# Kernel optimization log

Hardware: AMD Instinct MI355X
Metric: run time of the kernel (lower is better)

## Reference

```python
import jax, jax.numpy as jnp
import numpy as np

B, T, H, LAT, ADIM = 8192, 40, 100, 10, 2
ATT_TEMP = 5.0


def setup_inputs() -> dict:
    key = jax.random.key(0)
    ks = jax.random.split(key, 12)
    return {
        "sampled_att_z": jax.random.normal(ks[0], (B, LAT), jnp.float32),
        "enc_h": jax.random.normal(ks[1], (B, H), jnp.float32),
        # keep IDM params strictly positive / physically plausible to avoid inf
        "idm_params": 1.0 + 2.0 * jax.random.uniform(ks[2], (B, 5), jnp.float32),
        "idm_s": jax.random.uniform(ks[3], (B, T, 8), jnp.float32),
        "sdv_acts": jax.random.normal(ks[4], (B, T, ADIM), jnp.float32),
        "linear_W": jax.random.normal(ks[5], (LAT, H), jnp.float32) / np.float32(np.sqrt(LAT)),
        "linear_b": jnp.zeros((H,), jnp.float32),
        "lstm_Wx": jax.random.normal(ks[6], (H + ADIM, 4 * H), jnp.float32) / np.float32(np.sqrt(H + ADIM)),
        "lstm_Wh": jax.random.normal(ks[7], (H, 4 * H), jnp.float32) / np.float32(np.sqrt(H)),
        "lstm_b": jnp.zeros((4 * H,), jnp.float32),
        "att_W": jax.random.normal(ks[8], (H, 1), jnp.float32) / np.float32(np.sqrt(H)),
        "att_b": jnp.zeros((1,), jnp.float32),
        # precomputed per-step noise, replacing tf.random.normal inside the loop
        "noise_f": jax.random.normal(ks[9], (T, B, 1), jnp.float32),
        "noise_m": jax.random.normal(ks[10], (T, B, 1), jnp.float32),
    }


def reference(sampled_att_z, enc_h, idm_params, idm_s, sdv_acts,
              linear_W, linear_b, lstm_Wx, lstm_Wh, lstm_b, att_W, att_b,
              noise_f, noise_m):
    desired_v = idm_params[:, 0:1]
    desired_tgap = idm_params[:, 1:2]
    min_jamx = idm_params[:, 2:3]
    max_act = idm_params[:, 3:4]
    min_act = idm_params[:, 4:5]

    def idm_driver(vel, dv, dx):  # all [B,1]
        dx = jnp.clip(dx, 0.5, 1000.0)
        desired_gap = min_jamx + jax.nn.relu(
            desired_tgap * vel + vel * dv / (2.0 * jnp.sqrt(max_act * min_act)))
        act = max_act * (1.0 - (vel / desired_v) ** 4 - (desired_gap / dx) ** 2)
        return jnp.clip(act, -3.0, 3.0)

    att_proj = sampled_att_z @ linear_W + linear_b  # [B,H]; also the att_context and init h,c

    s_tm = jnp.swapaxes(idm_s, 0, 1)      # [T,B,8]
    a_tm = jnp.swapaxes(sdv_acts, 0, 1)   # [T,B,ADIM]

    ego_v0 = idm_s[:, 0, 0:1]
    ego_x0 = idm_s[:, 0, 3:4]
    zero_act = jnp.zeros_like(ego_v0)  # step-0 kinematic update is a no-op

    def step(carry, xs):
        ego_v, ego_x, h, c, act = carry
        s, sdv, nf, nm = xs
        ego_v = ego_v + act * 0.1
        ego_x = ego_x + ego_v * 0.1 + 0.5 * act * 0.1 ** 2

        f_v, m_v = s[:, 1:2], s[:, 2:3]
        f_x, m_x = s[:, 4:5], s[:, 5:6]
        f_ex, m_ex = s[:, 6:7], s[:, 7:8]

        ef_act = idm_driver(ego_v, ego_v - f_v, f_x - ego_x)
        ef_act = f_ex * ef_act + (1.0 - f_ex) * nf
        em_act = idm_driver(ego_v, ego_v - m_v, m_x - ego_x)
        em_act = m_ex * em_act + (1.0 - m_ex) * nm

        x_in = jnp.concatenate([att_proj, sdv], axis=-1)  # [B,H+ADIM]
        z = x_in @ lstm_Wx + h @ lstm_Wh + lstm_b          # [B,4H], keras gate order i,f,g,o
        zi, zf, zg, zo = jnp.split(z, 4, axis=-1)
        c = jax.nn.sigmoid(zf) * c + jax.nn.sigmoid(zi) * jnp.tanh(zg)
        h = jax.nn.sigmoid(zo) * jnp.tanh(c)

        att_score = jax.nn.sigmoid(ATT_TEMP * (h @ att_W + att_b))  # [B,1]
        act = (1.0 - att_score) * ef_act + att_score * em_act
        return (ego_v, ego_x, h, c, act), (act, att_score)

    init = (ego_v0, ego_x0, att_proj, att_proj, zero_act)
    _, (acts, atts) = jax.lax.scan(step, init, (s_tm, a_tm, noise_f, noise_m))
    act_seq = jnp.swapaxes(acts, 0, 1)  # [B,T,1]
    att_seq = jnp.swapaxes(atts, 0, 1)  # [B,T,1]
    return act_seq, att_seq
```

## Files before the change

### kernel.cpp

```cpp
#include <hip/hip_runtime.h>
#include <math.h>


#define B_TOT 8192
#define T_STEPS 40
#define NB 16

typedef _Float16 f16;
typedef f16 f16x8 __attribute__((ext_vector_type(8)));
typedef float f32x4 __attribute__((ext_vector_type(4)));

__device__ __forceinline__ float rcpf(float x) { return __builtin_amdgcn_rcpf(x); }
__device__ __forceinline__ float ex2(float x)  { return __builtin_amdgcn_exp2f(x); }
__device__ __forceinline__ float sigf(float x)  { return rcpf(1.f + ex2(-1.44269504f * x)); }
__device__ __forceinline__ float tanhf_(float x){ return fmaf(-2.f, rcpf(1.f + ex2(2.88539008f * x)), 1.f); }


__global__ __launch_bounds__(256) void idm_prep(
    const float* __restrict__ Wx, const float* __restrict__ Wh,
    const float* __restrict__ bvec, const float* __restrict__ attw,
    f16* __restrict__ whb, f16* __restrict__ wxb,
    float* __restrict__ bp, f16* __restrict__ awb)
{
  int i = blockIdx.x * 256 + threadIdx.x;
  int k = i >> 9, n = i & 511;
  int g = n >> 7, j128 = n & 127;
  float vh = 0.f, vx = 0.f;
  if (j128 < 100) {
    int col = g * 100 + j128;
    if (k < 100)      { vh = Wh[k * 400 + col]; vx = Wx[k * 400 + col]; }
    else if (k < 102) { vh = Wx[k * 400 + col]; }
  }
  int idx = (((n >> 4) * 4 + (k >> 5)) * 64 + (((k >> 3) & 3) * 16 + (n & 15))) * 8 + (k & 7);
  whb[idx] = (f16)vh;
  wxb[idx] = (f16)vx;
  if (i < 512) { int gg = i >> 7, jj = i & 127; bp[i] = (jj < 100) ? bvec[gg * 100 + jj] : 0.f; }
  if (i < 2048) {
    int j = i & 7, l = (i >> 3) & 63, kf = i >> 9;
    int kk = kf * 32 + ((l >> 4) & 3) * 8 + j;
    int col = l & 15;
    awb[i] = (f16)((col == 0 && kk < 100) ? attw[kk] : 0.f);
  }
}

__global__ __launch_bounds__(448, 4) void idm_main(
    const float* __restrict__ z_att,
    const float* __restrict__ linear_W,
    const float* __restrict__ linear_b,
    const float* __restrict__ sdv_acts,
    const f16* __restrict__ whb, const f16* __restrict__ wxb,
    const float* __restrict__ bp, const f16* __restrict__ awbg,
    const float* __restrict__ idm_params,
    const float* __restrict__ idm_s,
    const float* __restrict__ att_b,
    const float* __restrict__ noise_f,
    const float* __restrict__ noise_m,
    float* __restrict__ out)
{
  __shared__ f16 hS[2][16][136];
  __shared__ f16 sdvS[T_STEPS][16][2];
  __shared__ float logitS[T_STEPS][16];

  const int tid = threadIdx.x;
  const int w  = tid >> 6;
  const int l  = tid & 63;
  const int lr = l & 15;
  const int lq = l >> 4;
  const int b0g = blockIdx.x * NB;
  const int jcol = 16 * w + lr;

  for (int idx = tid; idx < 2176; idx += 448) ((unsigned*)hS)[idx] = 0u;
  for (int idx = tid; idx < 1280; idx += 448) {
    float v = sdv_acts[(size_t)b0g * 80 + idx];
    int b = idx / 80, r = idx - b * 80;
    sdvS[r >> 1][b][r & 1] = (f16)v;
  }
  __syncthreads();

  if (tid < 256) {
    int b = tid >> 4, oct = tid & 15;
    float za[10];
    #pragma unroll
    for (int t2 = 0; t2 < 10; ++t2) za[t2] = z_att[(b0g + b) * 10 + t2];
    #pragma unroll
    for (int jj = 0; jj < 8; ++jj) {
      int j = oct * 8 + jj;
      if (j < 100) {
        float acc = linear_b[j];
        #pragma unroll
        for (int t2 = 0; t2 < 10; ++t2) acc = fmaf(za[t2], linear_W[t2 * 100 + j], acc);
        hS[0][b][j] = (f16)acc;
      }
    }
  }
  if (tid < 32) {
    int bb = tid >> 1, ii = tid & 1;
    hS[0][bb][100 + ii] = sdvS[0][bb][ii];
  }
  __syncthreads();

  f16x8 wb[4][4];
  #pragma unroll
  for (int g = 0; g < 4; ++g) {
    int tile = w + 8 * g;
    #pragma unroll
    for (int kf = 0; kf < 4; ++kf)
      wb[g][kf] = *(const f16x8*)(wxb + ((size_t)(tile * 4 + kf) * 64 + l) * 8);
  }
  f32x4 cx[4];
  #pragma unroll
  for (int g = 0; g < 4; ++g) {
    float bpv = bp[(w + 8 * g) * 16 + lr];
    f32x4 c = {bpv, bpv, bpv, bpv};
    cx[g] = c;
  }
  #pragma unroll
  for (int kf = 0; kf < 4; ++kf) {
    f16x8 a = *(const f16x8*)(&hS[0][lr][kf * 32 + lq * 8]);
    #pragma unroll
    for (int g = 0; g < 4; ++g)
      cx[g] = __builtin_amdgcn_mfma_f32_16x16x32_f16(a, wb[g][kf], cx[g], 0, 0, 0);
  }
  #pragma unroll
  for (int g = 0; g < 4; ++g) {
    int tile = w + 8 * g;
    #pragma unroll
    for (int kf = 0; kf < 4; ++kf)
      wb[g][kf] = *(const f16x8*)(whb + ((size_t)(tile * 4 + kf) * 64 + l) * 8);
  }
  f16x8 awb[4];
  #pragma unroll
  for (int kf = 0; kf < 4; ++kf)
    awb[kf] = *(const f16x8*)(awbg + ((size_t)kf * 64 + l) * 8);

  float cst[4];
  #pragma unroll
  for (int r = 0; r < 4; ++r) cst[r] = (float)hS[0][lq * 4 + r][jcol];

  int p = 0;
  for (int t = 0; t < T_STEPS; ++t) {
    f16x8 a0 = *(const f16x8*)(&hS[p][lr][0  + lq * 8]);
    f16x8 a1 = *(const f16x8*)(&hS[p][lr][32 + lq * 8]);
    f16x8 a2 = *(const f16x8*)(&hS[p][lr][64 + lq * 8]);
    f16x8 a3 = *(const f16x8*)(&hS[p][lr][96 + lq * 8]);
    f32x4 z0 = cx[0], z1 = cx[1], z2 = cx[2], z3 = cx[3];
    z0 = __builtin_amdgcn_mfma_f32_16x16x32_f16(a0, wb[0][0], z0, 0, 0, 0);
    z1 = __builtin_amdgcn_mfma_f32_16x16x32_f16(a0, wb[1][0], z1, 0, 0, 0);
    z2 = __builtin_amdgcn_mfma_f32_16x16x32_f16(a0, wb[2][0], z2, 0, 0, 0);
    z3 = __builtin_amdgcn_mfma_f32_16x16x32_f16(a0, wb[3][0], z3, 0, 0, 0);
    z0 = __builtin_amdgcn_mfma_f32_16x16x32_f16(a1, wb[0][1], z0, 0, 0, 0);
    z1 = __builtin_amdgcn_mfma_f32_16x16x32_f16(a1, wb[1][1], z1, 0, 0, 0);
    z2 = __builtin_amdgcn_mfma_f32_16x16x32_f16(a1, wb[2][1], z2, 0, 0, 0);
    z3 = __builtin_amdgcn_mfma_f32_16x16x32_f16(a1, wb[3][1], z3, 0, 0, 0);
    z0 = __builtin_amdgcn_mfma_f32_16x16x32_f16(a2, wb[0][2], z0, 0, 0, 0);
    z1 = __builtin_amdgcn_mfma_f32_16x16x32_f16(a2, wb[1][2], z1, 0, 0, 0);
    z2 = __builtin_amdgcn_mfma_f32_16x16x32_f16(a2, wb[2][2], z2, 0, 0, 0);
    z3 = __builtin_amdgcn_mfma_f32_16x16x32_f16(a2, wb[3][2], z3, 0, 0, 0);
    z0 = __builtin_amdgcn_mfma_f32_16x16x32_f16(a3, wb[0][3], z0, 0, 0, 0);
    z1 = __builtin_amdgcn_mfma_f32_16x16x32_f16(a3, wb[1][3], z1, 0, 0, 0);
    z2 = __builtin_amdgcn_mfma_f32_16x16x32_f16(a3, wb[2][3], z2, 0, 0, 0);
    z3 = __builtin_amdgcn_mfma_f32_16x16x32_f16(a3, wb[3][3], z3, 0, 0, 0);

    if (w == 0) {
      f32x4 zA = {0.f, 0.f, 0.f, 0.f};
      zA = __builtin_amdgcn_mfma_f32_16x16x32_f16(a0, awb[0], zA, 0, 0, 0);
      zA = __builtin_amdgcn_mfma_f32_16x16x32_f16(a1, awb[1], zA, 0, 0, 0);
      zA = __builtin_amdgcn_mfma_f32_16x16x32_f16(a2, awb[2], zA, 0, 0, 0);
      zA = __builtin_amdgcn_mfma_f32_16x16x32_f16(a3, awb[3], zA, 0, 0, 0);
      if (t > 0 && lr == 0) {
        #pragma unroll
        for (int r = 0; r < 4; ++r) logitS[t - 1][lq * 4 + r] = zA[r];
      }
    }

    #pragma unroll
    for (int r = 0; r < 4; ++r) {
      float si = sigf(z0[r]);
      float sf = sigf(z1[r]);
      float tg = tanhf_(z2[r]);
      float so = sigf(z3[r]);
      float cc = fmaf(sf, cst[r], si * tg);
      float hh = so * tanhf_(cc);
      cst[r] = cc;
      if (jcol < 100) hS[p ^ 1][lq * 4 + r][jcol] = (f16)hh;
    }
    if (t + 1 < T_STEPS && tid < 32) {
      int bb = tid >> 1, ii = tid & 1;
      hS[p ^ 1][bb][100 + ii] = sdvS[t + 1][bb][ii];
    }
    __syncthreads();
    p ^= 1;
  }

  if (w == 0) {
    f16x8 a0 = *(const f16x8*)(&hS[p][lr][0  + lq * 8]);
    f16x8 a1 = *(const f16x8*)(&hS[p][lr][32 + lq * 8]);
    f16x8 a2 = *(const f16x8*)(&hS[p][lr][64 + lq * 8]);
    f16x8 a3 = *(const f16x8*)(&hS[p][lr][96 + lq * 8]);
    f32x4 zA = {0.f, 0.f, 0.f, 0.f};
    zA = __builtin_amdgcn_mfma_f32_16x16x32_f16(a0, awb[0], zA, 0, 0, 0);
    zA = __builtin_amdgcn_mfma_f32_16x16x32_f16(a1, awb[1], zA, 0, 0, 0);
    zA = __builtin_amdgcn_mfma_f32_16x16x32_f16(a2, awb[2], zA, 0, 0, 0);
    zA = __builtin_amdgcn_mfma_f32_16x16x32_f16(a3, awb[3], zA, 0, 0, 0);
    if (lr == 0) {
      #pragma unroll
      for (int r = 0; r < 4; ++r) logitS[T_STEPS - 1][lq * 4 + r] = zA[r];
    }
  }
  __syncthreads();

  if (tid < 16) {
    int b = b0g + tid;
    const float* P = idm_params + (size_t)b * 5;
    float des_v = P[0], des_tg = P[1], min_jx = P[2], max_a = P[3];
    float inv2s = 0.5f / sqrtf(max_a * P[4]);
    float inv_dv = rcpf(des_v);
    float ego_v = idm_s[(size_t)b * T_STEPS * 8 + 0];
    float ego_x = idm_s[(size_t)b * T_STEPS * 8 + 3];
    float attb = att_b[0];
    float act = 0.f;
    for (int t = 0; t < T_STEPS; ++t) {
      const float* s = idm_s + ((size_t)b * T_STEPS + t) * 8;
      float4 s03 = *(const float4*)(s);
      float4 s47 = *(const float4*)(s + 4);
      float nf = noise_f[(size_t)t * B_TOT + b];
      float nm = noise_m[(size_t)t * B_TOT + b];
      float lg = attb + logitS[t][tid];

      ego_v += act * 0.1f;
      ego_x += ego_v * 0.1f + act * 0.005f;
      float f_v = s03.y, m_v = s03.z, f_x = s47.x, m_x = s47.y, f_ex = s47.z, m_ex = s47.w;
      float af_, am_;
      {
        float dx = fminf(fmaxf(f_x - ego_x, 0.5f), 1000.f);
        float dg = min_jx + fmaxf(0.f, des_tg * ego_v + ego_v * (ego_v - f_v) * inv2s);
        float r = ego_v * inv_dv; float r2 = r * r; float q = dg * rcpf(dx);
        af_ = fminf(fmaxf(max_a * (1.f - r2 * r2 - q * q), -3.f), 3.f);
      }
      {
        float dx = fminf(fmaxf(m_x - ego_x, 0.5f), 1000.f);
        float dg = min_jx + fmaxf(0.f, des_tg * ego_v + ego_v * (ego_v - m_v) * inv2s);
        float r = ego_v * inv_dv; float r2 = r * r; float q = dg * rcpf(dx);
        am_ = fminf(fmaxf(max_a * (1.f - r2 * r2 - q * q), -3.f), 3.f);
      }
      float ef2 = f_ex * af_ + (1.f - f_ex) * nf;
      float em2 = m_ex * am_ + (1.f - m_ex) * nm;
      float att = sigf(5.f * lg);
      act = (1.f - att) * ef2 + att * em2;
      out[(size_t)b * T_STEPS + t] = act;
      out[(size_t)B_TOT * T_STEPS + (size_t)b * T_STEPS + t] = att;
    }
  }
}

extern "C" void kernel_launch(void* const* d_in, const int* in_sizes, int n_in,
                              void* d_out, int out_size, void* d_ws, size_t ws_size,
                              hipStream_t stream) {
  const float* z_att      = (const float*)d_in[0];
  const float* idm_params = (const float*)d_in[2];
  const float* idm_s      = (const float*)d_in[3];
  const float* sdv_acts   = (const float*)d_in[4];
  const float* linear_W   = (const float*)d_in[5];
  const float* linear_b   = (const float*)d_in[6];
  const float* lstm_Wx    = (const float*)d_in[7];
  const float* lstm_Wh    = (const float*)d_in[8];
  const float* lstm_b     = (const float*)d_in[9];
  const float* att_W      = (const float*)d_in[10];
  const float* att_b      = (const float*)d_in[11];
  const float* noise_f    = (const float*)d_in[12];
  const float* noise_m    = (const float*)d_in[13];
  float* out = (float*)d_out;

  f16*   whb = (f16*)d_ws;
  f16*   wxb = (f16*)((char*)d_ws + 131072);
  float* bp  = (float*)((char*)d_ws + 262144);
  f16*   awb = (f16*)((char*)d_ws + 264192);

  idm_prep<<<256, 256, 0, stream>>>(lstm_Wx, lstm_Wh, lstm_b, att_W, whb, wxb, bp, awb);
  idm_main<<<B_TOT / NB, 448, 0, stream>>>(z_att, linear_W, linear_b, sdv_acts,
                                           whb, wxb, bp, awb,
                                           idm_params, idm_s, att_b,
                                           noise_f, noise_m, out);
}
```

Measured before the change: 192.7 us.

## Split LSTM gate tiles across 14 waves with smem transpose for cell update

Doubles the block to 896 threads so each wave holds two gate tiles instead of four, writes the gate pre-activations to a shared transpose buffer, and lets every thread compute the cell update for one hidden unit across two batch rows. The aim is to cut per-wave serial MFMA and transcendental work inside the 40-step recurrence. The IDM inputs, noise and attention weights are now staged in shared memory, and outputs are written back as coalesced vectors. In exchange there is a second barrier per step, much more LDS use, and a single h buffer in place of the double buffer.

```diff
diff --git a/kernel.cpp b/kernel.cpp
--- a/kernel.cpp
+++ b/kernel.cpp
@@ -43,7 +43,7 @@
   }
 }
 
-__global__ __launch_bounds__(448, 4) void idm_main(
+__global__ __launch_bounds__(896, 7) void idm_main(
     const float* __restrict__ z_att,
     const float* __restrict__ linear_W,
     const float* __restrict__ linear_b,
@@ -57,9 +57,14 @@
     const float* __restrict__ noise_m,
     float* __restrict__ out)
 {
-  __shared__ f16 hS[2][16][136];
-  __shared__ f16 sdvS[T_STEPS][16][2];
+  __shared__ f16   hS[16][136];
+  __shared__ float zT[496][20];
   __shared__ float logitS[T_STEPS][16];
+  __shared__ f16   sdvS[T_STEPS][16][2];
+  __shared__ float sS[16][T_STEPS][6];
+  __shared__ float nS[2][T_STEPS][16];
+  __shared__ float accS[2][16][T_STEPS];
+  __shared__ f16   awbS[2048];
 
   const int tid = threadIdx.x;
   const int w  = tid >> 6;
@@ -67,14 +72,33 @@
   const int lr = l & 15;
   const int lq = l >> 4;
   const int b0g = blockIdx.x * NB;
-  const int jcol = 16 * w + lr;
-
-  for (int idx = tid; idx < 2176; idx += 448) ((unsigned*)hS)[idx] = 0u;
-  for (int idx = tid; idx < 1280; idx += 448) {
+  const int i1 = 2 * w, i2 = 2 * w + 1;
+  const int T1 = (i1 / 7) * 8 + (i1 % 7);
+  const int T2 = (i2 / 7) * 8 + (i2 % 7);
+  const int gj = tid >> 3;
+  const int gb = (tid & 7) * 2;
+
+  for (int idx = tid; idx < 1088; idx += 896) ((unsigned*)hS)[idx] = 0u;
+  for (int idx = tid; idx < 1280; idx += 896) {
     float v = sdv_acts[(size_t)b0g * 80 + idx];
     int b = idx / 80, r = idx - b * 80;
     sdvS[r >> 1][b][r & 1] = (f16)v;
   }
+  for (int idx = tid; idx < 5120; idx += 896) {
+    int f = idx & 7;
+    if (f != 0 && f != 3) {
+      int b = idx / 320, rem = idx - b * 320, t = rem >> 3;
+      sS[b][t][(f < 3) ? f - 1 : f - 2] = idm_s[(size_t)b0g * 320 + idx];
+    }
+  }
+  for (int idx = tid; idx < 1280; idx += 896) {
+    int which = idx >= 640 ? 1 : 0;
+    int r = idx - which * 640;
+    int t = r >> 4, i = r & 15;
+    nS[which][t][i] = which ? noise_m[(size_t)t * B_TOT + b0g + i]
+                            : noise_f[(size_t)t * B_TOT + b0g + i];
+  }
+  for (int idx = tid; idx < 1024; idx += 896) ((unsigned*)awbS)[idx] = ((const unsigned*)awbg)[idx];
   __syncthreads();
 
   if (tid < 256) {
@@ -89,122 +113,89 @@
         float acc = linear_b[j];
         #pragma unroll
         for (int t2 = 0; t2 < 10; ++t2) acc = fmaf(za[t2], linear_W[t2 * 100 + j], acc);
-        hS[0][b][j] = (f16)acc;
-      }
-    }
-  }
-  if (tid < 32) {
-    int bb = tid >> 1, ii = tid & 1;
-    hS[0][bb][100 + ii] = sdvS[0][bb][ii];
-  }
-  __syncthreads();
-
-  f16x8 wb[4][4];
-  #pragma unroll
-  for (int g = 0; g < 4; ++g) {
-    int tile = w + 8 * g;
-    #pragma unroll
-    for (int kf = 0; kf < 4; ++kf)
-      wb[g][kf] = *(const f16x8*)(wxb + ((size_t)(tile * 4 + kf) * 64 + l) * 8);
-  }
-  f32x4 cx[4];
-  #pragma unroll
-  for (int g = 0; g < 4; ++g) {
-    float bpv = bp[(w + 8 * g) * 16 + lr];
-    f32x4 c = {bpv, bpv, bpv, bpv};
-    cx[g] = c;
-  }
+        hS[b][j] = (f16)acc;
+      }
+    }
+  }
+  if (tid < 32) hS[tid >> 1][100 + (tid & 1)] = sdvS[0][tid >> 1][tid & 1];
+  __syncthreads();
+
+  f16x8 wbA[4], wbB[4];
   #pragma unroll
   for (int kf = 0; kf < 4; ++kf) {
-    f16x8 a = *(const f16x8*)(&hS[0][lr][kf * 32 + lq * 8]);
-    #pragma unroll
-    for (int g = 0; g < 4; ++g)
-      cx[g] = __builtin_amdgcn_mfma_f32_16x16x32_f16(a, wb[g][kf], cx[g], 0, 0, 0);
-  }
+    wbA[kf] = *(const f16x8*)(wxb + ((size_t)(T1 * 4 + kf) * 64 + l) * 8);
+    wbB[kf] = *(const f16x8*)(wxb + ((size_t)(T2 * 4 + kf) * 64 + l) * 8);
+  }
+  float bpA = bp[T1 * 16 + lr], bpB = bp[T2 * 16 + lr];
+  f32x4 cxA = {bpA, bpA, bpA, bpA};
+  f32x4 cxB = {bpB, bpB, bpB, bpB};
   #pragma unroll
-  for (int g = 0; g < 4; ++g) {
-    int tile = w + 8 * g;
-    #pragma unroll
-    for (int kf = 0; kf < 4; ++kf)
-      wb[g][kf] = *(const f16x8*)(whb + ((size_t)(tile * 4 + kf) * 64 + l) * 8);
-  }
-  f16x8 awb[4];
+  for (int kf = 0; kf < 4; ++kf) {
+    f16x8 a = *(const f16x8*)(&hS[lr][kf * 32 + lq * 8]);
+    cxA = __builtin_amdgcn_mfma_f32_16x16x32_f16(a, wbA[kf], cxA, 0, 0, 0);
+    cxB = __builtin_amdgcn_mfma_f32_16x16x32_f16(a, wbB[kf], cxB, 0, 0, 0);
+  }
   #pragma unroll
-  for (int kf = 0; kf < 4; ++kf)
-    awb[kf] = *(const f16x8*)(awbg + ((size_t)kf * 64 + l) * 8);
-
-  float cst[4];
-  #pragma unroll
-  for (int r = 0; r < 4; ++r) cst[r] = (float)hS[0][lq * 4 + r][jcol];
-
-  int p = 0;
+  for (int kf = 0; kf < 4; ++kf) {
+    wbA[kf] = *(const f16x8*)(whb + ((size_t)(T1 * 4 + kf) * 64 + l) * 8);
+    wbB[kf] = *(const f16x8*)(whb + ((size_t)(T2 * 4 + kf) * 64 + l) * 8);
+  }
+
+  float cst0 = 0.f, cst1 = 0.f;
+  const bool glive = (gj < 100);
+  if (glive) { cst0 = (float)hS[gb][gj]; cst1 = (float)hS[gb + 1][gj]; }
+
+  #pragma unroll 1
   for (int t = 0; t < T_STEPS; ++t) {
-    f16x8 a0 = *(const f16x8*)(&hS[p][lr][0  + lq * 8]);
-    f16x8 a1 = *(const f16x8*)(&hS[p][lr][32 + lq * 8]);
-    f16x8 a2 = *(const f16x8*)(&hS[p][lr][64 + lq * 8]);
-    f16x8 a3 = *(const f16x8*)(&hS[p][lr][96 + lq * 8]);
-    f32x4 z0 = cx[0], z1 = cx[1], z2 = cx[2], z3 = cx[3];
-    z0 = __builtin_amdgcn_mfma_f32_16x16x32_f16(a0, wb[0][0], z0, 0, 0, 0);
-    z1 = __builtin_amdgcn_mfma_f32_16x16x32_f16(a0, wb[1][0], z1, 0, 0, 0);
-    z2 = __builtin_amdgcn_mfma_f32_16x16x32_f16(a0, wb[2][0], z2, 0, 0, 0);
-    z3 = __builtin_amdgcn_mfma_f32_16x16x32_f16(a0, wb[3][0], z3, 0, 0, 0);
-    z0 = __builtin_amdgcn_mfma_f32_16x16x32_f16(a1, wb[0][1], z0, 0, 0, 0);
-    z1 = __builtin_amdgcn_mfma_f32_16x16x32_f16(a1, wb[1][1], z1, 0, 0, 0);
-    z2 = __builtin_amdgcn_mfma_f32_16x16x32_f16(a1, wb[2][1], z2, 0, 0, 0);
-    z3 = __builtin_amdgcn_mfma_f32_16x16x32_f16(a1, wb[3][1], z3, 0, 0, 0);
-    z0 = __builtin_amdgcn_mfma_f32_16x16x32_f16(a2, wb[0][2], z0, 0, 0, 0);
-    z1 = __builtin_amdgcn_mfma_f32_16x16x32_f16(a2, wb[1][2], z1, 0, 0, 0);
-    z2 = __builtin_amdgcn_mfma_f32_16x16x32_f16(a2, wb[2][2], z2, 0, 0, 0);
-    z3 = __builtin_amdgcn_mfma_f32_16x16x32_f16(a2, wb[3][2], z3, 0, 0, 0);
-    z0 = __builtin_amdgcn_mfma_f32_16x16x32_f16(a3, wb[0][3], z0, 0, 0, 0);
-    z1 = __builtin_amdgcn_mfma_f32_16x16x32_f16(a3, wb[1][3], z1, 0, 0, 0);
-    z2 = __builtin_amdgcn_mfma_f32_16x16x32_f16(a3, wb[2][3], z2, 0, 0, 0);
-    z3 = __builtin_amdgcn_mfma_f32_16x16x32_f16(a3, wb[3][3], z3, 0, 0, 0);
-
-    if (w == 0) {
-      f32x4 zA = {0.f, 0.f, 0.f, 0.f};
-      zA = __builtin_amdgcn_mfma_f32_16x16x32_f16(a0, awb[0], zA, 0, 0, 0);
-      zA = __builtin_amdgcn_mfma_f32_16x16x32_f16(a1, awb[1], zA, 0, 0, 0);
-      zA = __builtin_amdgcn_mfma_f32_16x16x32_f16(a2, awb[2], zA, 0, 0, 0);
-      zA = __builtin_amdgcn_mfma_f32_16x16x32_f16(a3, awb[3], zA, 0, 0, 0);
-      if (t > 0 && lr == 0) {
-        #pragma unroll
-        for (int r = 0; r < 4; ++r) logitS[t - 1][lq * 4 + r] = zA[r];
-      }
-    }
-
-    #pragma unroll
-    for (int r = 0; r < 4; ++r) {
-      float si = sigf(z0[r]);
-      float sf = sigf(z1[r]);
-      float tg = tanhf_(z2[r]);
-      float so = sigf(z3[r]);
-      float cc = fmaf(sf, cst[r], si * tg);
-      float hh = so * tanhf_(cc);
-      cst[r] = cc;
-      if (jcol < 100) hS[p ^ 1][lq * 4 + r][jcol] = (f16)hh;
-    }
-    if (t + 1 < T_STEPS && tid < 32) {
-      int bb = tid >> 1, ii = tid & 1;
-      hS[p ^ 1][bb][100 + ii] = sdvS[t + 1][bb][ii];
-    }
+    f32x4 zA = cxA, zB = cxB;
+    f32x4 zL = {0.f, 0.f, 0.f, 0.f};
+    #pragma unroll
+    for (int kf = 0; kf < 4; ++kf) {
+      f16x8 a = *(const f16x8*)(&hS[lr][kf * 32 + lq * 8]);
+      zA = __builtin_amdgcn_mfma_f32_16x16x32_f16(a, wbA[kf], zA, 0, 0, 0);
+      zB = __builtin_amdgcn_mfma_f32_16x16x32_f16(a, wbB[kf], zB, 0, 0, 0);
+      if (w == 0) {
+        f16x8 af = *(const f16x8*)(awbS + ((size_t)kf * 64 + l) * 8);
+        zL = __builtin_amdgcn_mfma_f32_16x16x32_f16(a, af, zL, 0, 0, 0);
+      }
+    }
+    if (w == 0 && t > 0 && lr == 0) {
+      #pragma unroll
+      for (int r = 0; r < 4; ++r) logitS[t - 1][lq * 4 + r] = zL[r];
+    }
+    *(f32x4*)&zT[T1 * 16 + lr][lq * 4] = zA;
+    *(f32x4*)&zT[T2 * 16 + lr][lq * 4] = zB;
     __syncthreads();
-    p ^= 1;
+
+    if (glive) {
+      float2 zi = *(const float2*)&zT[0 * 128 + gj][gb];
+      float2 zf = *(const float2*)&zT[1 * 128 + gj][gb];
+      float2 zg = *(const float2*)&zT[2 * 128 + gj][gb];
+      float2 zo = *(const float2*)&zT[3 * 128 + gj][gb];
+      float cc0 = fmaf(sigf(zf.x), cst0, sigf(zi.x) * tanhf_(zg.x));
+      float hh0 = sigf(zo.x) * tanhf_(cc0);
+      float cc1 = fmaf(sigf(zf.y), cst1, sigf(zi.y) * tanhf_(zg.y));
+      float hh1 = sigf(zo.y) * tanhf_(cc1);
+      cst0 = cc0; cst1 = cc1;
+      hS[gb][gj]     = (f16)hh0;
+      hS[gb + 1][gj] = (f16)hh1;
+    }
+    if (t + 1 < T_STEPS && tid < 32)
+      hS[tid >> 1][100 + (tid & 1)] = sdvS[t + 1][tid >> 1][tid & 1];
+    __syncthreads();
   }
 
   if (w == 0) {
-    f16x8 a0 = *(const f16x8*)(&hS[p][lr][0  + lq * 8]);
-    f16x8 a1 = *(const f16x8*)(&hS[p][lr][32 + lq * 8]);
-    f16x8 a2 = *(const f16x8*)(&hS[p][lr][64 + lq * 8]);
-    f16x8 a3 = *(const f16x8*)(&hS[p][lr][96 + lq * 8]);
-    f32x4 zA = {0.f, 0.f, 0.f, 0.f};
-    zA = __builtin_amdgcn_mfma_f32_16x16x32_f16(a0, awb[0], zA, 0, 0, 0);
-    zA = __builtin_amdgcn_mfma_f32_16x16x32_f16(a1, awb[1], zA, 0, 0, 0);
-    zA = __builtin_amdgcn_mfma_f32_16x16x32_f16(a2, awb[2], zA, 0, 0, 0);
-    zA = __builtin_amdgcn_mfma_f32_16x16x32_f16(a3, awb[3], zA, 0, 0, 0);
+    f32x4 zL = {0.f, 0.f, 0.f, 0.f};
+    #pragma unroll
+    for (int kf = 0; kf < 4; ++kf) {
+      f16x8 a  = *(const f16x8*)(&hS[lr][kf * 32 + lq * 8]);
+      f16x8 af = *(const f16x8*)(awbS + ((size_t)kf * 64 + l) * 8);
+      zL = __builtin_amdgcn_mfma_f32_16x16x32_f16(a, af, zL, 0, 0, 0);
+    }
     if (lr == 0) {
       #pragma unroll
-      for (int r = 0; r < 4; ++r) logitS[T_STEPS - 1][lq * 4 + r] = zA[r];
+      for (int r = 0; r < 4; ++r) logitS[T_STEPS - 1][lq * 4 + r] = zL[r];
     }
   }
   __syncthreads();
@@ -215,41 +206,47 @@
     float des_v = P[0], des_tg = P[1], min_jx = P[2], max_a = P[3];
     float inv2s = 0.5f / sqrtf(max_a * P[4]);
     float inv_dv = rcpf(des_v);
-    float ego_v = idm_s[(size_t)b * T_STEPS * 8 + 0];
-    float ego_x = idm_s[(size_t)b * T_STEPS * 8 + 3];
+    float ego_v = idm_s[(size_t)b * 320 + 0];
+    float ego_x = idm_s[(size_t)b * 320 + 3];
     float attb = att_b[0];
     float act = 0.f;
+    #pragma unroll 4
     for (int t = 0; t < T_STEPS; ++t) {
-      const float* s = idm_s + ((size_t)b * T_STEPS + t) * 8;
-      float4 s03 = *(const float4*)(s);
-      float4 s47 = *(const float4*)(s + 4);
-      float nf = noise_f[(size_t)t * B_TOT + b];
-      float nm = noise_m[(size_t)t * B_TOT + b];
+      float2 s01 = *(const float2*)&sS[tid][t][0];
+      float2 s23 = *(const float2*)&sS[tid][t][2];
+      float2 s45 = *(const float2*)&sS[tid][t][4];
+      float nf = nS[0][t][tid], nm = nS[1][t][tid];
       float lg = attb + logitS[t][tid];
-
       ego_v += act * 0.1f;
       ego_x += ego_v * 0.1f + act * 0.005f;
-      float f_v = s03.y, m_v = s03.z, f_x = s47.x, m_x = s47.y, f_ex = s47.z, m_ex = s47.w;
       float af_, am_;
       {
-        float dx = fminf(fmaxf(f_x - ego_x, 0.5f), 1000.f);
-        float dg = min_jx + fmaxf(0.f, des_tg * ego_v + ego_v * (ego_v - f_v) * inv2s);
+        float dx = fminf(fmaxf(s23.x - ego_x, 0.5f), 1000.f);
+        float dg = min_jx + fmaxf(0.f, des_tg * ego_v + ego_v * (ego_v - s01.x) * inv2s);
         float r = ego_v * inv_dv; float r2 = r * r; float q = dg * rcpf(dx);
         af_ = fminf(fmaxf(max_a * (1.f - r2 * r2 - q * q), -3.f), 3.f);
       }
       {
-        float dx = fminf(fmaxf(m_x - ego_x, 0.5f), 1000.f);
-        float dg = min_jx + fmaxf(0.f, des_tg * ego_v + ego_v * (ego_v - m_v) * inv2s);
+        float dx = fminf(fmaxf(s23.y - ego_x, 0.5f), 1000.f);
+        float dg = min_jx + fmaxf(0.f, des_tg * ego_v + ego_v * (ego_v - s01.y) * inv2s);
         float r = ego_v * inv_dv; float r2 = r * r; float q = dg * rcpf(dx);
         am_ = fminf(fmaxf(max_a * (1.f - r2 * r2 - q * q), -3.f), 3.f);
       }
-      float ef2 = f_ex * af_ + (1.f - f_ex) * nf;
-      float em2 = m_ex * am_ + (1.f - m_ex) * nm;
+      float ef2 = s45.x * af_ + (1.f - s45.x) * nf;
+      float em2 = s45.y * am_ + (1.f - s45.y) * nm;
       float att = sigf(5.f * lg);
       act = (1.f - att) * ef2 + att * em2;
-      out[(size_t)b * T_STEPS + t] = act;
-      out[(size_t)B_TOT * T_STEPS + (size_t)b * T_STEPS + t] = att;
-    }
+      accS[0][tid][t] = act;
+      accS[1][tid][t] = att;
+    }
+  }
+  __syncthreads();
+
+  if (tid < 160) {
+    f32x4 va = ((const f32x4*)&accS[0][0][0])[tid];
+    f32x4 vt = ((const f32x4*)&accS[1][0][0])[tid];
+    *(f32x4*)(out + (size_t)b0g * T_STEPS + tid * 4) = va;
+    *(f32x4*)(out + (size_t)B_TOT * T_STEPS + (size_t)b0g * T_STEPS + tid * 4) = vt;
   }
 }
 
@@ -277,7 +274,7 @@
   f16*   awb = (f16*)((char*)d_ws + 264192);
 
   idm_prep<<<256, 256, 0, stream>>>(lstm_Wx, lstm_Wh, lstm_b, att_W, whb, wxb, bp, awb);
-  idm_main<<<B_TOT / NB, 448, 0, stream>>>(z_att, linear_W, linear_b, sdv_acts,
+  idm_main<<<B_TOT / NB, 896, 0, stream>>>(z_att, linear_W, linear_b, sdv_acts,
                                            whb, wxb, bp, awb,
                                            idm_params, idm_s, att_b,
                                            noise_f, noise_m, out);
```

After: 245.6 us. +27.5%, slower.

## Fold attention logit into padded gate column and stage IDM inputs in LDS

Applied to the files above, without the earlier changes.

The attention weight vector is packed into an unused padding column (n=100) of the Wh tile, so the logit comes out of the existing gate MFMA for wave 6. This removes the separate per-step attention MFMA chain on wave 0. The IDM state and noise are prefetched cooperatively into shared memory before the recurrence, and outputs are buffered in LDS and written with coalesced vector stores instead of scattered per-thread global stores. The cost is extra LDS use, which may lower occupancy.

```diff
diff --git a/kernel.cpp b/kernel.cpp
--- a/kernel.cpp
+++ b/kernel.cpp
@@ -20,7 +20,7 @@
     const float* __restrict__ Wx, const float* __restrict__ Wh,
     const float* __restrict__ bvec, const float* __restrict__ attw,
     f16* __restrict__ whb, f16* __restrict__ wxb,
-    float* __restrict__ bp, f16* __restrict__ awb)
+    float* __restrict__ bp)
 {
   int i = blockIdx.x * 256 + threadIdx.x;
   int k = i >> 9, n = i & 511;
@@ -30,17 +30,13 @@
     int col = g * 100 + j128;
     if (k < 100)      { vh = Wh[k * 400 + col]; vx = Wx[k * 400 + col]; }
     else if (k < 102) { vh = Wx[k * 400 + col]; }
+  } else if (n == 100 && k < 100) {
+    vh = attw[k];
   }
   int idx = (((n >> 4) * 4 + (k >> 5)) * 64 + (((k >> 3) & 3) * 16 + (n & 15))) * 8 + (k & 7);
   whb[idx] = (f16)vh;
   wxb[idx] = (f16)vx;
   if (i < 512) { int gg = i >> 7, jj = i & 127; bp[i] = (jj < 100) ? bvec[gg * 100 + jj] : 0.f; }
-  if (i < 2048) {
-    int j = i & 7, l = (i >> 3) & 63, kf = i >> 9;
-    int kk = kf * 32 + ((l >> 4) & 3) * 8 + j;
-    int col = l & 15;
-    awb[i] = (f16)((col == 0 && kk < 100) ? attw[kk] : 0.f);
-  }
 }
 
 __global__ __launch_bounds__(448, 4) void idm_main(
@@ -49,7 +45,7 @@
     const float* __restrict__ linear_b,
     const float* __restrict__ sdv_acts,
     const f16* __restrict__ whb, const f16* __restrict__ wxb,
-    const float* __restrict__ bp, const f16* __restrict__ awbg,
+    const float* __restrict__ bp,
     const float* __restrict__ idm_params,
     const float* __restrict__ idm_s,
     const float* __restrict__ att_b,
@@ -57,9 +53,12 @@
     const float* __restrict__ noise_m,
     float* __restrict__ out)
 {
-  __shared__ f16 hS[2][16][136];
-  __shared__ f16 sdvS[T_STEPS][16][2];
+  __shared__ f16   hS[2][16][136];
+  __shared__ f16   sdvS[T_STEPS][16][2];
   __shared__ float logitS[T_STEPS][16];
+  __shared__ float sS[16][T_STEPS][6];
+  __shared__ float nS[2][T_STEPS][16];
+  __shared__ float accS[2][16][T_STEPS];
 
   const int tid = threadIdx.x;
   const int w  = tid >> 6;
@@ -74,6 +73,20 @@
     float v = sdv_acts[(size_t)b0g * 80 + idx];
     int b = idx / 80, r = idx - b * 80;
     sdvS[r >> 1][b][r & 1] = (f16)v;
+  }
+  for (int idx = tid; idx < 5120; idx += 448) {
+    int f = idx & 7;
+    if (f != 0 && f != 3) {
+      int b = idx / 320, rem = idx - b * 320, t = rem >> 3;
+      sS[b][t][(f < 3) ? f - 1 : f - 2] = idm_s[(size_t)b0g * 320 + idx];
+    }
+  }
+  for (int idx = tid; idx < 1280; idx += 448) {
+    int which = idx >= 640 ? 1 : 0;
+    int r = idx - which * 640;
+    int t = r >> 4, i = r & 15;
+    nS[which][t][i] = which ? noise_m[(size_t)t * B_TOT + b0g + i]
+                            : noise_f[(size_t)t * B_TOT + b0g + i];
   }
   __syncthreads();
 
@@ -93,10 +106,7 @@
       }
     }
   }
-  if (tid < 32) {
-    int bb = tid >> 1, ii = tid & 1;
-    hS[0][bb][100 + ii] = sdvS[0][bb][ii];
-  }
+  if (tid < 32) hS[0][tid >> 1][100 + (tid & 1)] = sdvS[0][tid >> 1][tid & 1];
   __syncthreads();
 
   f16x8 wb[4][4];
@@ -128,10 +138,6 @@
     for (int kf = 0; kf < 4; ++kf)
       wb[g][kf] = *(const f16x8*)(whb + ((size_t)(tile * 4 + kf) * 64 + l) * 8);
   }
-  f16x8 awb[4];
-  #pragma unroll
-  for (int kf = 0; kf < 4; ++kf)
-    awb[kf] = *(const f16x8*)(awbg + ((size_t)kf * 64 + l) * 8);
 
   float cst[4];
   #pragma unroll
@@ -161,16 +167,9 @@
     z2 = __builtin_amdgcn_mfma_f32_16x16x32_f16(a3, wb[2][3], z2, 0, 0, 0);
     z3 = __builtin_amdgcn_mfma_f32_16x16x32_f16(a3, wb[3][3], z3, 0, 0, 0);
 
-    if (w == 0) {
-      f32x4 zA = {0.f, 0.f, 0.f, 0.f};
-      zA = __builtin_amdgcn_mfma_f32_16x16x32_f16(a0, awb[0], zA, 0, 0, 0);
-      zA = __builtin_amdgcn_mfma_f32_16x16x32_f16(a1, awb[1], zA, 0, 0, 0);
-      zA = __builtin_amdgcn_mfma_f32_16x16x32_f16(a2, awb[2], zA, 0, 0, 0);
-      zA = __builtin_amdgcn_mfma_f32_16x16x32_f16(a3, awb[3], zA, 0, 0, 0);
-      if (t > 0 && lr == 0) {
-        #pragma unroll
-        for (int r = 0; r < 4; ++r) logitS[t - 1][lq * 4 + r] = zA[r];
-      }
+    if (w == 6 && t > 0 && lr == 4) {
+      #pragma unroll
+      for (int r = 0; r < 4; ++r) logitS[t - 1][lq * 4 + r] = z0[r];
     }
 
     #pragma unroll
@@ -184,27 +183,22 @@
       cst[r] = cc;
       if (jcol < 100) hS[p ^ 1][lq * 4 + r][jcol] = (f16)hh;
     }
-    if (t + 1 < T_STEPS && tid < 32) {
-      int bb = tid >> 1, ii = tid & 1;
-      hS[p ^ 1][bb][100 + ii] = sdvS[t + 1][bb][ii];
-    }
+    if (t + 1 < T_STEPS && tid < 32)
+      hS[p ^ 1][tid >> 1][100 + (tid & 1)] = sdvS[t + 1][tid >> 1][tid & 1];
     __syncthreads();
     p ^= 1;
   }
 
-  if (w == 0) {
-    f16x8 a0 = *(const f16x8*)(&hS[p][lr][0  + lq * 8]);
-    f16x8 a1 = *(const f16x8*)(&hS[p][lr][32 + lq * 8]);
-    f16x8 a2 = *(const f16x8*)(&hS[p][lr][64 + lq * 8]);
-    f16x8 a3 = *(const f16x8*)(&hS[p][lr][96 + lq * 8]);
-    f32x4 zA = {0.f, 0.f, 0.f, 0.f};
-    zA = __builtin_amdgcn_mfma_f32_16x16x32_f16(a0, awb[0], zA, 0, 0, 0);
-    zA = __builtin_amdgcn_mfma_f32_16x16x32_f16(a1, awb[1], zA, 0, 0, 0);
-    zA = __builtin_amdgcn_mfma_f32_16x16x32_f16(a2, awb[2], zA, 0, 0, 0);
-    zA = __builtin_amdgcn_mfma_f32_16x16x32_f16(a3, awb[3], zA, 0, 0, 0);
-    if (lr == 0) {
+  if (w == 6) {
+    f32x4 zL = {0.f, 0.f, 0.f, 0.f};
+    #pragma unroll
+    for (int kf = 0; kf < 4; ++kf) {
+      f16x8 a = *(const f16x8*)(&hS[p][lr][kf * 32 + lq * 8]);
+      zL = __builtin_amdgcn_mfma_f32_16x16x32_f16(a, wb[0][kf], zL, 0, 0, 0);
+    }
+    if (lr == 4) {
       #pragma unroll
-      for (int r = 0; r < 4; ++r) logitS[T_STEPS - 1][lq * 4 + r] = zA[r];
+      for (int r = 0; r < 4; ++r) logitS[T_STEPS - 1][lq * 4 + r] = zL[r];
     }
   }
   __syncthreads();
@@ -215,41 +209,47 @@
     float des_v = P[0], des_tg = P[1], min_jx = P[2], max_a = P[3];
     float inv2s = 0.5f / sqrtf(max_a * P[4]);
     float inv_dv = rcpf(des_v);
-    float ego_v = idm_s[(size_t)b * T_STEPS * 8 + 0];
-    float ego_x = idm_s[(size_t)b * T_STEPS * 8 + 3];
+    float ego_v = idm_s[(size_t)b * 320 + 0];
+    float ego_x = idm_s[(size_t)b * 320 + 3];
     float attb = att_b[0];
     float act = 0.f;
+    #pragma unroll 4
     for (int t = 0; t < T_STEPS; ++t) {
-      const float* s = idm_s + ((size_t)b * T_STEPS + t) * 8;
-      float4 s03 = *(const float4*)(s);
-      float4 s47 = *(const float4*)(s + 4);
-      float nf = noise_f[(size_t)t * B_TOT + b];
-      float nm = noise_m[(size_t)t * B_TOT + b];
+      float2 s01 = *(const float2*)&sS[tid][t][0];
+      float2 s23 = *(const float2*)&sS[tid][t][2];
+      float2 s45 = *(const float2*)&sS[tid][t][4];
+      float nf = nS[0][t][tid], nm = nS[1][t][tid];
       float lg = attb + logitS[t][tid];
-
       ego_v += act * 0.1f;
       ego_x += ego_v * 0.1f + act * 0.005f;
-      float f_v = s03.y, m_v = s03.z, f_x = s47.x, m_x = s47.y, f_ex = s47.z, m_ex = s47.w;
       float af_, am_;
       {
-        float dx = fminf(fmaxf(f_x - ego_x, 0.5f), 1000.f);
-        float dg = min_jx + fmaxf(0.f, des_tg * ego_v + ego_v * (ego_v - f_v) * inv2s);
+        float dx = fminf(fmaxf(s23.x - ego_x, 0.5f), 1000.f);
+        float dg = min_jx + fmaxf(0.f, des_tg * ego_v + ego_v * (ego_v - s01.x) * inv2s);
         float r = ego_v * inv_dv; float r2 = r * r; float q = dg * rcpf(dx);
         af_ = fminf(fmaxf(max_a * (1.f - r2 * r2 - q * q), -3.f), 3.f);
       }
       {
-        float dx = fminf(fmaxf(m_x - ego_x, 0.5f), 1000.f);
-        float dg = min_jx + fmaxf(0.f, des_tg * ego_v + ego_v * (ego_v - m_v) * inv2s);
+        float dx = fminf(fmaxf(s23.y - ego_x, 0.5f), 1000.f);
+        float dg = min_jx + fmaxf(0.f, des_tg * ego_v + ego_v * (ego_v - s01.y) * inv2s);
         float r = ego_v * inv_dv; float r2 = r * r; float q = dg * rcpf(dx);
         am_ = fminf(fmaxf(max_a * (1.f - r2 * r2 - q * q), -3.f), 3.f);
       }
-      float ef2 = f_ex * af_ + (1.f - f_ex) * nf;
-      float em2 = m_ex * am_ + (1.f - m_ex) * nm;
+      float ef2 = s45.x * af_ + (1.f - s45.x) * nf;
+      float em2 = s45.y * am_ + (1.f - s45.y) * nm;
       float att = sigf(5.f * lg);
       act = (1.f - att) * ef2 + att * em2;
-      out[(size_t)b * T_STEPS + t] = act;
-      out[(size_t)B_TOT * T_STEPS + (size_t)b * T_STEPS + t] = att;
-    }
+      accS[0][tid][t] = act;
+      accS[1][tid][t] = att;
+    }
+  }
+  __syncthreads();
+
+  if (tid < 160) {
+    f32x4 va = ((const f32x4*)&accS[0][0][0])[tid];
+    f32x4 vt = ((const f32x4*)&accS[1][0][0])[tid];
+    *(f32x4*)(out + (size_t)b0g * T_STEPS + tid * 4) = va;
+    *(f32x4*)(out + (size_t)B_TOT * T_STEPS + (size_t)b0g * T_STEPS + tid * 4) = vt;
   }
 }
 
@@ -274,11 +274,10 @@
   f16*   whb = (f16*)d_ws;
   f16*   wxb = (f16*)((char*)d_ws + 131072);
   float* bp  = (float*)((char*)d_ws + 262144);
-  f16*   awb = (f16*)((char*)d_ws + 264192);
-
-  idm_prep<<<256, 256, 0, stream>>>(lstm_Wx, lstm_Wh, lstm_b, att_W, whb, wxb, bp, awb);
+
+  idm_prep<<<256, 256, 0, stream>>>(lstm_Wx, lstm_Wh, lstm_b, att_W, whb, wxb, bp);
   idm_main<<<B_TOT / NB, 448, 0, stream>>>(z_att, linear_W, linear_b, sdv_acts,
-                                           whb, wxb, bp, awb,
+                                           whb, wxb, bp,
                                            idm_params, idm_s, att_b,
                                            noise_f, noise_m, out);
 }
```

Result: faster. 178.4 us (median of 2 runs) (-7.4%).
